# Performance work log

Hardware: AMD Instinct MI355X
Metric: run time of the kernel (lower is better)

The kernel has to match this reference:

```python
import jax, jax.numpy as jnp
import numpy as np

H = 8          # attention heads
HID = 256      # hidden dim
C = HID // H   # per-head channels
N = 50000      # nodes per node type
E = 500000     # edges per edge type
LRELU_SLOPE = 0.2
EPS_SOFTMAX = 1e-16
EPS_LN = 1e-5


def _gat(x_src, x_dst, ei, W, a_s, a_d, b, n_dst):
    # PyG GATConv (shared lin for src/dst since in_channels is int), concat heads
    h_src = (x_src @ W).reshape(-1, H, C)   # (Nsrc, H, C)
    h_dst = (x_dst @ W).reshape(-1, H, C)   # (Ndst, H, C)
    al_s = (h_src * a_s).sum(-1)            # (Nsrc, H)
    al_d = (h_dst * a_d).sum(-1)            # (Ndst, H)
    src, dst = ei[0], ei[1]
    alpha = jax.nn.leaky_relu(al_s[src] + al_d[dst], LRELU_SLOPE)  # (E, H)
    # segment softmax over edges grouped by destination node
    amax = jax.ops.segment_max(alpha, dst, num_segments=n_dst)
    amax = jnp.where(jnp.isfinite(amax), amax, 0.0)
    ex = jnp.exp(alpha - amax[dst])
    den = jax.ops.segment_sum(ex, dst, num_segments=n_dst)
    w = ex / (den[dst] + EPS_SOFTMAX)
    msg = h_src[src] * w[:, :, None]        # (E, H, C)
    out = jax.ops.segment_sum(msg, dst, num_segments=n_dst)
    return out.reshape(n_dst, HID) + b


def _ln(x, g, b):
    mu = x.mean(-1, keepdims=True)
    var = x.var(-1, keepdims=True)
    return (x - mu) / jnp.sqrt(var + EPS_LN) * g + b


def setup_inputs() -> dict:
    key = jax.random.key(0)
    ks = jax.random.split(key, 24)
    s = 1.0 / np.sqrt(HID)
    d = {}
    d["x_gene"] = jax.random.normal(ks[0], (N, HID), jnp.float32)
    d["x_pheno"] = jax.random.normal(ks[1], (N, HID), jnp.float32)
    d["ei_gp"] = jax.random.randint(ks[2], (2, E), 0, N, jnp.int32)
    d["ei_pg"] = jax.random.randint(ks[3], (2, E), 0, N, jnp.int32)
    d["ei_gg"] = jax.random.randint(ks[4], (2, E), 0, N, jnp.int32)
    i = 5
    for tag in ["gp", "pg", "gg"]:
        d[f"W_{tag}"] = jax.random.normal(ks[i], (HID, HID), jnp.float32) * s; i += 1
        d[f"a_s_{tag}"] = jax.random.normal(ks[i], (H, C), jnp.float32) * s; i += 1
        d[f"a_d_{tag}"] = jax.random.normal(ks[i], (H, C), jnp.float32) * s; i += 1
        d[f"b_{tag}"] = jnp.zeros((HID,), jnp.float32); i += 1
    d["ln_g_gene"] = jnp.ones((HID,), jnp.float32)
    d["ln_b_gene"] = jnp.zeros((HID,), jnp.float32)
    d["ln_g_ph"] = jnp.ones((HID,), jnp.float32)
    d["ln_b_ph"] = jnp.zeros((HID,), jnp.float32)
    return d


def reference(x_gene, x_pheno, ei_gp, ei_pg, ei_gg,
              W_gp, a_s_gp, a_d_gp, b_gp,
              W_pg, a_s_pg, a_d_pg, b_pg,
              W_gg, a_s_gg, a_d_gg, b_gg,
              ln_g_gene, ln_b_gene, ln_g_ph, ln_b_ph):
    # HeteroConv aggr='sum': sum conv outputs per destination node type
    out_gene = (_gat(x_pheno, x_gene, ei_pg, W_pg, a_s_pg, a_d_pg, b_pg, N)
                + _gat(x_gene, x_gene, ei_gg, W_gg, a_s_gg, a_d_gg, b_gg, N))
    out_ph = _gat(x_gene, x_pheno, ei_gp, W_gp, a_s_gp, a_d_gp, b_gp, N)
    # residual + layernorm (dropout is identity in eval / p=0)
    out_gene = _ln(out_gene + x_gene, ln_g_gene, ln_b_gene)
    out_ph = _ln(out_ph + x_pheno, ln_g_ph, ln_b_ph)
    return (out_gene, out_ph)
```

## Files before the change

kernel.cpp:

```cpp
#include <hip/hip_runtime.h>

#define NN 50000
#define EE 500000
#define CAP 64

typedef unsigned int u32;
typedef unsigned short ushort;
typedef __attribute__((ext_vector_type(8))) short short8v;
typedef __attribute__((ext_vector_type(4))) float float4v;

__device__ __forceinline__ ushort f2b(float f) {
  u32 u = __float_as_uint(f);
  u32 r = (u + 0x7fffu + ((u >> 16) & 1u)) >> 16;
  return (ushort)r;
}
__device__ __forceinline__ u32 pk2(float a, float b) {
  return (u32)f2b(a) | ((u32)f2b(b) << 16);
}
__device__ __forceinline__ float bl(u32 q) { return __uint_as_float(q << 16); }
__device__ __forceinline__ float bh(u32 q) { return __uint_as_float(q & 0xffff0000u); }
__device__ __forceinline__ void gload16(const void* g, void* l) {
  __builtin_amdgcn_global_load_lds((const __attribute__((address_space(1))) void*)g,
                                   (__attribute__((address_space(3))) void*)l, 16, 0, 0);
}

__global__ void prep_kernel(const float* __restrict__ W_gp, const float* __restrict__ W_pg,
                            const float* __restrict__ W_gg,
                            const float* __restrict__ as_gp, const float* __restrict__ as_pg,
                            const float* __restrict__ as_gg,
                            const float* __restrict__ ad_gp, const float* __restrict__ ad_pg,
                            const float* __restrict__ ad_gg,
                            const float* __restrict__ xg, const float* __restrict__ xp,
                            ushort* __restrict__ WT, ushort* __restrict__ V6T,
                            ushort* __restrict__ xb, int* __restrict__ cnt3) {
  int b = blockIdx.x;
  int k = threadIdx.x;
  if (b < 256) {
    int n = b;
    WT[(size_t)0 * 65536 + n * 256 + k] = f2b(W_gp[k * 256 + n]);
    WT[(size_t)1 * 65536 + n * 256 + k] = f2b(W_pg[k * 256 + n]);
    WT[(size_t)2 * 65536 + n * 256 + k] = f2b(W_gg[k * 256 + n]);
    return;
  }
  if (b < 304) {
    int idx = b - 256;
    int g = idx >> 3, h = idx & 7;
    const float* W;
    const float* a;
    switch (g) {
      case 0: W = W_gp; a = as_gp; break;
      case 1: W = W_gg; a = as_gg; break;
      case 2: W = W_pg; a = ad_pg; break;
      case 3: W = W_gg; a = ad_gg; break;
      case 4: W = W_pg; a = as_pg; break;
      default: W = W_gp; a = ad_gp; break;
    }
    const float4* wrow = (const float4*)&W[(size_t)k * 256 + h * 32];
    const float4* arow = (const float4*)&a[h * 32];
    float s = 0.f;
#pragma unroll
    for (int q = 0; q < 8; ++q) {
      float4 wv = wrow[q];
      float4 av = arow[q];
      s += wv.x * av.x + wv.y * av.y + wv.z * av.z + wv.w * av.w;
    }
    V6T[(size_t)(g * 8 + h) * 256 + k] = f2b(s);
    return;
  }
  if (b == 304) {
#pragma unroll
    for (int col = 48; col < 64; ++col) V6T[(size_t)col * 256 + k] = 0;
    return;
  }
  int gid = (b - 305) * 256 + k;
  const int gstride = 2048 * 256;
  for (int j = gid; j < 3 * NN; j += gstride) cnt3[j] = 0;
  const int tot = 2 * NN * 64;
  for (int i = gid; i < tot; i += gstride) {
    const float* src = (i < NN * 64) ? xg + (size_t)i * 4 : xp + ((size_t)i - (size_t)NN * 64) * 4;
    float4 v = *(const float4*)src;
    ushort4 o;
    o.x = f2b(v.x); o.y = f2b(v.y); o.z = f2b(v.z); o.w = f2b(v.w);
    *(ushort4*)&xb[(size_t)i * 4] = o;
  }
}

__global__ __launch_bounds__(256) void fused_compute(
    const ushort* __restrict__ xb, const ushort* __restrict__ WT,
    const ushort* __restrict__ V6T, ushort* __restrict__ hb3,
    ushort* __restrict__ alsb, float* __restrict__ ald3,
    const int* __restrict__ e0, const int* __restrict__ e1, const int* __restrict__ e2,
    int* __restrict__ cnt3, ushort* __restrict__ srcs3) {
  __shared__ ushort smem[16384];
  const int tid = threadIdx.x;
  const int l = tid & 63, w = tid >> 6;
  const int rr = l & 15, kb = l >> 4;
  if (blockIdx.y == 0) {
    const int T = 391 * 256;
    const int base = blockIdx.x * 256 + tid;
#pragma unroll
    for (int it = 0; it < 15; ++it) {
      int i = base + it * T;
      if (i < 3 * EE) {
        int which = i >= 2 * EE ? 2 : (i >= EE ? 1 : 0);
        const int* ei = which == 0 ? e0 : (which == 1 ? e1 : e2);
        int e = i - which * EE;
        int d = ei[EE + e];
        int s = ei[e];
        int gslot = which * NN + d;
        int pos = atomicAdd(&cnt3[gslot], 1);
        if (pos < CAP) srcs3[(size_t)gslot * CAP + pos] = (ushort)s;
      }
    }
    return;
  }
  if (blockIdx.y < 7) {
    ushort* As = smem;
    ushort* Bs = smem + 8192;
    const int yy = blockIdx.y - 1;
    const int p = yy >> 1;
    const int c0 = (yy & 1) * 128;
    const ushort* x = xb + (p == 1 ? (size_t)NN * 256 : 0);
    const ushort* Wp = WT + (size_t)p * 65536 + (size_t)c0 * 256;
    ushort* hb = hb3 + (size_t)p * 12800000;
    const int r0 = blockIdx.x * 128;
    const int wm = w >> 1, wn = w & 1;
    float4v acc[4][4];
#pragma unroll
    for (int mi = 0; mi < 4; ++mi)
#pragma unroll
      for (int ni = 0; ni < 4; ++ni) acc[mi][ni] = (float4v){0.f, 0.f, 0.f, 0.f};
    const int r1 = tid >> 2, g1 = tid & 3;
    const int r2 = 64 + (tid >> 2), g2 = tid & 3;

#define STAGE(buf, k0)                                                               \
  {                                                                                  \
    gload16(&x[(size_t)(r0 + r1) * 256 + (k0) + g1 * 8], &As[(buf) * 4096 + tid * 8]); \
    gload16(&x[(size_t)(r0 + r2) * 256 + (k0) + g2 * 8], &As[(buf) * 4096 + (tid + 256) * 8]); \
    gload16(&Wp[(size_t)r1 * 256 + (k0) + g1 * 8], &Bs[(buf) * 4096 + tid * 8]);     \
    gload16(&Wp[(size_t)r2 * 256 + (k0) + g2 * 8], &Bs[(buf) * 4096 + (tid + 256) * 8]); \
  }

    STAGE(0, 0);
    __syncthreads();
#pragma unroll
    for (int k = 0; k < 8; ++k) {
      const int buf = k & 1;
      if (k < 7) STAGE(buf ^ 1, (k + 1) * 32);
      short8v af[4], bf[4];
#pragma unroll
      for (int t = 0; t < 4; ++t) {
        af[t] = *(const short8v*)&As[buf * 4096 + (wm * 64 + t * 16 + rr) * 32 + kb * 8];
        bf[t] = *(const short8v*)&Bs[buf * 4096 + (wn * 64 + t * 16 + rr) * 32 + kb * 8];
      }
#pragma unroll
      for (int mi = 0; mi < 4; ++mi)
#pragma unroll
        for (int ni = 0; ni < 4; ++ni)
          acc[mi][ni] = __builtin_amdgcn_mfma_f32_16x16x32_bf16(bf[ni], af[mi], acc[mi][ni], 0, 0, 0);
      __syncthreads();
    }
#undef STAGE
#pragma unroll
    for (int mi = 0; mi < 4; ++mi) {
      const int row = r0 + wm * 64 + mi * 16 + rr;
      if (row < NN) {
        ushort* hp = &hb[(size_t)row * 256 + c0 + wn * 64 + kb * 4];
#pragma unroll
        for (int ni = 0; ni < 4; ++ni) {
          uint2 o;
          o.x = pk2(acc[mi][ni][0], acc[mi][ni][1]);
          o.y = pk2(acc[mi][ni][2], acc[mi][ni][3]);
          *(uint2*)&hp[ni * 16] = o;
        }
      }
    }
    return;
  }
  ushort* As2 = smem;
  short8v bfv[8];
#pragma unroll
  for (int k = 0; k < 8; ++k) {
    uint4 q = *(const uint4*)&V6T[(size_t)(w * 16 + rr) * 256 + k * 32 + kb * 8];
    bfv[k] = *(short8v*)&q;
  }
  for (int t = 0; t < 4; ++t) {
    const int r0 = blockIdx.x * 256 + t * 64;
    gload16(&xb[(size_t)(r0 + (tid >> 2)) * 256 + (tid & 3) * 8], &As2[tid * 8]);
    __syncthreads();
    float4v acc[4];
#pragma unroll
    for (int mi = 0; mi < 4; ++mi) acc[mi] = (float4v){0.f, 0.f, 0.f, 0.f};
#pragma unroll
    for (int k = 0; k < 8; ++k) {
      const int buf = k & 1;
      if (k < 7)
        gload16(&xb[(size_t)(r0 + (tid >> 2)) * 256 + (k + 1) * 32 + (tid & 3) * 8],
                &As2[(buf ^ 1) * 2048 + tid * 8]);
#pragma unroll
      for (int mi = 0; mi < 4; ++mi) {
        short8v afv = *(const short8v*)&As2[buf * 2048 + (mi * 16 + rr) * 32 + kb * 8];
        acc[mi] = __builtin_amdgcn_mfma_f32_16x16x32_bf16(bfv[k], afv, acc[mi], 0, 0, 0);
      }
      __syncthreads();
    }
    const int g = w * 2 + (kb >> 1);
    const int idx = (kb & 1) * 4;
#pragma unroll
    for (int mi = 0; mi < 4; ++mi) {
      int grow = r0 + mi * 16 + rr;
      float4 val = make_float4(acc[mi][0], acc[mi][1], acc[mi][2], acc[mi][3]);
      if (grow < NN) {
        if (g == 0 || g == 1) {
          ushort* arr = alsb + (g == 0 ? 0 : 800000);
          uint2 o;
          o.x = pk2(val.x, val.y);
          o.y = pk2(val.z, val.w);
          *(uint2*)&arr[(size_t)grow * 8 + idx] = o;
        } else if (g == 2 || g == 3) {
          float* arr = ald3 + (g == 2 ? 400000 : 800000);
          *(float4*)&arr[(size_t)grow * 8 + idx] = val;
        }
      } else if (grow < 2 * NN) {
        int r = grow - NN;
        if (g == 4) {
          uint2 o;
          o.x = pk2(val.x, val.y);
          o.y = pk2(val.z, val.w);
          *(uint2*)&alsb[400000 + (size_t)r * 8 + idx] = o;
        } else if (g == 5) {
          *(float4*)&ald3[(size_t)r * 8 + idx] = val;
        }
      }
    }
  }
}

__global__ __launch_bounds__(256) void gat_gather_ln(
    const int* __restrict__ cnt3, const ushort* __restrict__ srcs3,
    const ushort* __restrict__ hb3, const ushort* __restrict__ alsb,
    const float* __restrict__ ald3, const ushort* __restrict__ xb,
    const float* __restrict__ b_gp, const float* __restrict__ b_pg,
    const float* __restrict__ b_gg,
    const float* __restrict__ lng_g, const float* __restrict__ lnb_g,
    const float* __restrict__ lng_p, const float* __restrict__ lnb_p,
    float* __restrict__ out) {
  __shared__ float exs[4][8][68];
  __shared__ int ssrc[4][64];
  const int l = threadIdx.x & 63;
  const int wv = threadIdx.x >> 6;
  const int slot = blockIdx.x * 4 + wv;
  if (slot >= 2 * NN) return;
  const bool gene = (slot < NN);
  const int d = gene ? slot : slot - NN;
  const int sl = l & 31;
  const int half = l >> 5;
  const int hh = sl >> 2;
  float vout[8] = {0.f, 0.f, 0.f, 0.f, 0.f, 0.f, 0.f, 0.f};
  const int nph = gene ? 2 : 1;
  for (int q = 0; q < nph; ++q) {
    const int phase = gene ? (1 + q) : 0;
    const int cslot = phase * NN + d;
    const ushort* hmat = hb3 + (size_t)phase * 12800000;
    const ushort* al_s = alsb + (size_t)phase * 400000;
    const float* al_d = ald3 + (size_t)phase * 400000;
    const int cnt = cnt3[cslot];
    if (cnt == 0) continue;
    const ushort* srow = srcs3 + (size_t)cslot * CAP;
    float4 ad0 = *(const float4*)&al_d[(size_t)d * 8];
    float4 ad1 = *(const float4*)&al_d[(size_t)d * 8 + 4];
    const float ald[8] = {ad0.x, ad0.y, ad0.z, ad0.w, ad1.x, ad1.y, ad1.z, ad1.w};
    float den = 0.f;
    float acc8[8] = {0.f, 0.f, 0.f, 0.f, 0.f, 0.f, 0.f, 0.f};
    const ushort* hrow = hmat + sl * 8;
    {
      float ex[8] = {0.f, 0.f, 0.f, 0.f, 0.f, 0.f, 0.f, 0.f};
      int s = 0;
      if (l < cnt) {
        s = srow[l];
        uint4 sq = *(const uint4*)&al_s[(size_t)s * 8];
        float a[8] = {bl(sq.x) + ald[0], bh(sq.x) + ald[1], bl(sq.y) + ald[2], bh(sq.y) + ald[3],
                      bl(sq.z) + ald[4], bh(sq.z) + ald[5], bl(sq.w) + ald[6], bh(sq.w) + ald[7]};
#pragma unroll
        for (int h = 0; h < 8; ++h) ex[h] = __expf(fmaxf(a[h], 0.2f * a[h]));
      }
      ssrc[wv][l] = s;
#pragma unroll
      for (int h = 0; h < 8; ++h) exs[wv][h][l] = ex[h];
      int chunkr = (cnt + 3) & ~3;
      for (int j = 0; j < chunkr; j += 4) {
        int ja = j + half, jb = j + 2 + half;
        int sa = ssrc[wv][ja], sb = ssrc[wv][jb];
        float wa = exs[wv][hh][ja], wb = exs[wv][hh][jb];
        uint4 pa = *(const uint4*)&hrow[(size_t)sa * 256];
        uint4 pb = *(const uint4*)&hrow[(size_t)sb * 256];
        den += wa + wb;
        acc8[0] += bl(pa.x) * wa + bl(pb.x) * wb;
        acc8[1] += bh(pa.x) * wa + bh(pb.x) * wb;
        acc8[2] += bl(pa.y) * wa + bl(pb.y) * wb;
        acc8[3] += bh(pa.y) * wa + bh(pb.y) * wb;
        acc8[4] += bl(pa.z) * wa + bl(pb.z) * wb;
        acc8[5] += bh(pa.z) * wa + bh(pb.z) * wb;
        acc8[6] += bl(pa.w) * wa + bl(pb.w) * wb;
        acc8[7] += bh(pa.w) * wa + bh(pb.w) * wb;
      }
    }
#pragma unroll
    for (int i = 0; i < 8; ++i) acc8[i] += __shfl_xor(acc8[i], 32);
    den += __shfl_xor(den, 32);
    float wd = 1.f / (den + 1e-16f);
#pragma unroll
    for (int i = 0; i < 8; ++i) vout[i] += acc8[i] * wd;
  }
  const ushort* xrow = xb + (gene ? 0 : (size_t)NN * 256) + (size_t)d * 256;
  uint4 xq = *(const uint4*)&xrow[sl * 8];
  float4 ba, bb;
  if (gene) {
    float4 p1 = *(const float4*)&b_pg[sl * 8];
    float4 p2 = *(const float4*)&b_pg[sl * 8 + 4];
    float4 q1 = *(const float4*)&b_gg[sl * 8];
    float4 q2 = *(const float4*)&b_gg[sl * 8 + 4];
    ba = make_float4(p1.x + q1.x, p1.y + q1.y, p1.z + q1.z, p1.w + q1.w);
    bb = make_float4(p2.x + q2.x, p2.y + q2.y, p2.z + q2.z, p2.w + q2.w);
  } else {
    ba = *(const float4*)&b_gp[sl * 8];
    bb = *(const float4*)&b_gp[sl * 8 + 4];
  }
  vout[0] += bl(xq.x) + ba.x; vout[1] += bh(xq.x) + ba.y;
  vout[2] += bl(xq.y) + ba.z; vout[3] += bh(xq.y) + ba.w;
  vout[4] += bl(xq.z) + bb.x; vout[5] += bh(xq.z) + bb.y;
  vout[6] += bl(xq.w) + bb.z; vout[7] += bh(xq.w) + bb.w;
  float s = 0.f, ss = 0.f;
#pragma unroll
  for (int i = 0; i < 8; ++i) { s += vout[i]; ss += vout[i] * vout[i]; }
#pragma unroll
  for (int off = 1; off < 32; off <<= 1) {
    s += __shfl_xor(s, off);
    ss += __shfl_xor(ss, off);
  }
  float mu = s * (1.f / 256.f);
  float var = ss * (1.f / 256.f) - mu * mu;
  float rstd = rsqrtf(var + 1e-5f);
  const float* lg = gene ? lng_g : lng_p;
  const float* lb = gene ? lnb_g : lnb_p;
  float4 g1 = *(const float4*)&lg[sl * 8];
  float4 g2 = *(const float4*)&lg[sl * 8 + 4];
  float4 c1 = *(const float4*)&lb[sl * 8];
  float4 c2 = *(const float4*)&lb[sl * 8 + 4];
  if (half == 0) {
    float* op = &out[(size_t)slot * 256 + sl * 8];
    float4 o1 = make_float4((vout[0] - mu) * rstd * g1.x + c1.x,
                            (vout[1] - mu) * rstd * g1.y + c1.y,
                            (vout[2] - mu) * rstd * g1.z + c1.z,
                            (vout[3] - mu) * rstd * g1.w + c1.w);
    float4 o2 = make_float4((vout[4] - mu) * rstd * g2.x + c2.x,
                            (vout[5] - mu) * rstd * g2.y + c2.y,
                            (vout[6] - mu) * rstd * g2.z + c2.z,
                            (vout[7] - mu) * rstd * g2.w + c2.w);
    *(float4*)op = o1;
    *(float4*)(op + 4) = o2;
  }
}

extern "C" void kernel_launch(void* const* d_in, const int* in_sizes, int n_in,
                              void* d_out, int out_size, void* d_ws, size_t ws_size,
                              hipStream_t stream) {
  const float* x_gene = (const float*)d_in[0];
  const float* x_pheno = (const float*)d_in[1];
  const int* ei_gp = (const int*)d_in[2];
  const int* ei_pg = (const int*)d_in[3];
  const int* ei_gg = (const int*)d_in[4];
  const float* W_gp = (const float*)d_in[5];
  const float* a_s_gp = (const float*)d_in[6];
  const float* a_d_gp = (const float*)d_in[7];
  const float* b_gp = (const float*)d_in[8];
  const float* W_pg = (const float*)d_in[9];
  const float* a_s_pg = (const float*)d_in[10];
  const float* a_d_pg = (const float*)d_in[11];
  const float* b_pg = (const float*)d_in[12];
  const float* W_gg = (const float*)d_in[13];
  const float* a_s_gg = (const float*)d_in[14];
  const float* a_d_gg = (const float*)d_in[15];
  const float* b_gg = (const float*)d_in[16];
  const float* ln_g_gene = (const float*)d_in[17];
  const float* ln_b_gene = (const float*)d_in[18];
  const float* ln_g_ph = (const float*)d_in[19];
  const float* ln_b_ph = (const float*)d_in[20];
  float* out = (float*)d_out;

  float* ws = (float*)d_ws;
  ushort* hb3 = (ushort*)ws;
  ushort* xb = (ushort*)(ws + 19200000);
  ushort* alsb = (ushort*)(ws + 32060000);
  float* ald3 = ws + 32700000;
  ushort* WT = (ushort*)(ws + 33960000);
  ushort* V6T = (ushort*)(ws + 34060000);
  int* ibase = (int*)(ws + 34080000);
  int* cnt3 = ibase;
  ushort* srcs3 = (ushort*)(ibase + 150016);

  prep_kernel<<<305 + 2048, 256, 0, stream>>>(
      W_gp, W_pg, W_gg, a_s_gp, a_s_pg, a_s_gg, a_d_gp, a_d_pg, a_d_gg,
      x_gene, x_pheno, WT, V6T, xb, cnt3);

  fused_compute<<<dim3(391, 8), 256, 0, stream>>>(xb, WT, V6T, hb3, alsb, ald3,
                                                  ei_gp, ei_pg, ei_gg, cnt3, srcs3);

  gat_gather_ln<<<(2 * NN + 3) / 4, 256, 0, stream>>>(
      cnt3, srcs3, hb3, alsb, ald3, xb, b_gp, b_pg, b_gg,
      ln_g_gene, ln_b_gene, ln_g_ph, ln_b_ph, out);
}
```

Baseline: 298.8 us.

## Move edge bucketing into prep kernel and zero counters with memset

Measured after the change: 336.5 us. +12.6%, slower.

```diff
diff --git a/kernel.cpp b/kernel.cpp
--- a/kernel.cpp
+++ b/kernel.cpp
@@ -31,8 +31,11 @@
                             const float* __restrict__ ad_gp, const float* __restrict__ ad_pg,
                             const float* __restrict__ ad_gg,
                             const float* __restrict__ xg, const float* __restrict__ xp,
+                            const int* __restrict__ e0, const int* __restrict__ e1,
+                            const int* __restrict__ e2,
                             ushort* __restrict__ WT, ushort* __restrict__ V6T,
-                            ushort* __restrict__ xb, int* __restrict__ cnt3) {
+                            ushort* __restrict__ xb, int* __restrict__ cnt3,
+                            ushort* __restrict__ srcs3) {
   int b = blockIdx.x;
   int k = threadIdx.x;
   if (b < 256) {
@@ -72,52 +75,43 @@
     for (int col = 48; col < 64; ++col) V6T[(size_t)col * 256 + k] = 0;
     return;
   }
-  int gid = (b - 305) * 256 + k;
-  const int gstride = 2048 * 256;
-  for (int j = gid; j < 3 * NN; j += gstride) cnt3[j] = 0;
-  const int tot = 2 * NN * 64;
-  for (int i = gid; i < tot; i += gstride) {
-    const float* src = (i < NN * 64) ? xg + (size_t)i * 4 : xp + ((size_t)i - (size_t)NN * 64) * 4;
-    float4 v = *(const float4*)src;
-    ushort4 o;
-    o.x = f2b(v.x); o.y = f2b(v.y); o.z = f2b(v.z); o.w = f2b(v.w);
-    *(ushort4*)&xb[(size_t)i * 4] = o;
-  }
-}
-
-__global__ __launch_bounds__(256) void fused_compute(
+  if (b < 2353) {
+    int i = (b - 305) * 256 + k;
+    const int gstride = 2048 * 256;
+    const int tot = 2 * NN * 64;
+    for (; i < tot; i += gstride) {
+      const float* src = (i < NN * 64) ? xg + (size_t)i * 4 : xp + ((size_t)i - (size_t)NN * 64) * 4;
+      float4 v = *(const float4*)src;
+      ushort4 o;
+      o.x = f2b(v.x); o.y = f2b(v.y); o.z = f2b(v.z); o.w = f2b(v.w);
+      *(ushort4*)&xb[(size_t)i * 4] = o;
+    }
+    return;
+  }
+  int i = (b - 2353) * 256 + k;
+  if (i >= 3 * EE) return;
+  int which = i >= 2 * EE ? 2 : (i >= EE ? 1 : 0);
+  const int* ei = which == 0 ? e0 : (which == 1 ? e1 : e2);
+  int e = i - which * EE;
+  int d = ei[EE + e];
+  int s = ei[e];
+  int gslot = which * NN + d;
+  int pos = atomicAdd(&cnt3[gslot], 1);
+  if (pos < CAP) srcs3[(size_t)gslot * CAP + pos] = (ushort)s;
+}
+
+__global__ __launch_bounds__(256) void compute_kernel(
     const ushort* __restrict__ xb, const ushort* __restrict__ WT,
     const ushort* __restrict__ V6T, ushort* __restrict__ hb3,
-    ushort* __restrict__ alsb, float* __restrict__ ald3,
-    const int* __restrict__ e0, const int* __restrict__ e1, const int* __restrict__ e2,
-    int* __restrict__ cnt3, ushort* __restrict__ srcs3) {
+    ushort* __restrict__ alsb, float* __restrict__ ald3) {
   __shared__ ushort smem[16384];
   const int tid = threadIdx.x;
   const int l = tid & 63, w = tid >> 6;
   const int rr = l & 15, kb = l >> 4;
-  if (blockIdx.y == 0) {
-    const int T = 391 * 256;
-    const int base = blockIdx.x * 256 + tid;
-#pragma unroll
-    for (int it = 0; it < 15; ++it) {
-      int i = base + it * T;
-      if (i < 3 * EE) {
-        int which = i >= 2 * EE ? 2 : (i >= EE ? 1 : 0);
-        const int* ei = which == 0 ? e0 : (which == 1 ? e1 : e2);
-        int e = i - which * EE;
-        int d = ei[EE + e];
-        int s = ei[e];
-        int gslot = which * NN + d;
-        int pos = atomicAdd(&cnt3[gslot], 1);
-        if (pos < CAP) srcs3[(size_t)gslot * CAP + pos] = (ushort)s;
-      }
-    }
-    return;
-  }
-  if (blockIdx.y < 7) {
+  if (blockIdx.y < 6) {
     ushort* As = smem;
     ushort* Bs = smem + 8192;
-    const int yy = blockIdx.y - 1;
+    const int yy = blockIdx.y;
     const int p = yy >> 1;
     const int c0 = (yy & 1) * 128;
     const ushort* x = xb + (p == 1 ? (size_t)NN * 256 : 0);
@@ -399,12 +393,14 @@
   int* cnt3 = ibase;
   ushort* srcs3 = (ushort*)(ibase + 150016);
 
-  prep_kernel<<<305 + 2048, 256, 0, stream>>>(
+  const int e3blk = (3 * EE + 255) / 256;
+
+  hipMemsetAsync(cnt3, 0, 150016 * 4, stream);
+  prep_kernel<<<2353 + e3blk, 256, 0, stream>>>(
       W_gp, W_pg, W_gg, a_s_gp, a_s_pg, a_s_gg, a_d_gp, a_d_pg, a_d_gg,
-      x_gene, x_pheno, WT, V6T, xb, cnt3);
-
-  fused_compute<<<dim3(391, 8), 256, 0, stream>>>(xb, WT, V6T, hb3, alsb, ald3,
-                                                  ei_gp, ei_pg, ei_gg, cnt3, srcs3);
+      x_gene, x_pheno, ei_gp, ei_pg, ei_gg, WT, V6T, xb, cnt3, srcs3);
+
+  compute_kernel<<<dim3(391, 7), 256, 0, stream>>>(xb, WT, V6T, hb3, alsb, ald3);
 
   gat_gather_ln<<<(2 * NN + 3) / 4, 256, 0, stream>>>(
       cnt3, srcs3, hb3, alsb, ald3, xb, b_gp, b_pg, b_gg,
```

## Fuse fp32-to-bf16 input conversion into GEMM staging and drop xb buffer

Applied to the files above, without the earlier changes.

Result: no change. 299.7 us (+0.3%).

```diff
diff --git a/kernel.cpp b/kernel.cpp
--- a/kernel.cpp
+++ b/kernel.cpp
@@ -30,9 +30,7 @@
                             const float* __restrict__ as_gg,
                             const float* __restrict__ ad_gp, const float* __restrict__ ad_pg,
                             const float* __restrict__ ad_gg,
-                            const float* __restrict__ xg, const float* __restrict__ xp,
-                            ushort* __restrict__ WT, ushort* __restrict__ V6T,
-                            ushort* __restrict__ xb, int* __restrict__ cnt3) {
+                            ushort* __restrict__ WT, ushort* __restrict__ V6T) {
   int b = blockIdx.x;
   int k = threadIdx.x;
   if (b < 256) {
@@ -67,28 +65,14 @@
     V6T[(size_t)(g * 8 + h) * 256 + k] = f2b(s);
     return;
   }
-  if (b == 304) {
-#pragma unroll
-    for (int col = 48; col < 64; ++col) V6T[(size_t)col * 256 + k] = 0;
-    return;
-  }
-  int gid = (b - 305) * 256 + k;
-  const int gstride = 2048 * 256;
-  for (int j = gid; j < 3 * NN; j += gstride) cnt3[j] = 0;
-  const int tot = 2 * NN * 64;
-  for (int i = gid; i < tot; i += gstride) {
-    const float* src = (i < NN * 64) ? xg + (size_t)i * 4 : xp + ((size_t)i - (size_t)NN * 64) * 4;
-    float4 v = *(const float4*)src;
-    ushort4 o;
-    o.x = f2b(v.x); o.y = f2b(v.y); o.z = f2b(v.z); o.w = f2b(v.w);
-    *(ushort4*)&xb[(size_t)i * 4] = o;
-  }
-}
-
-__global__ __launch_bounds__(256) void fused_compute(
-    const ushort* __restrict__ xb, const ushort* __restrict__ WT,
-    const ushort* __restrict__ V6T, ushort* __restrict__ hb3,
-    ushort* __restrict__ alsb, float* __restrict__ ald3,
+#pragma unroll
+  for (int col = 48; col < 64; ++col) V6T[(size_t)col * 256 + k] = 0;
+}
+
+__global__ __launch_bounds__(256) void mega_compute(
+    const float* __restrict__ xg, const float* __restrict__ xp,
+    const ushort* __restrict__ WT, const ushort* __restrict__ V6T,
+    ushort* __restrict__ hb3, ushort* __restrict__ alsb, float* __restrict__ ald3,
     const int* __restrict__ e0, const int* __restrict__ e1, const int* __restrict__ e2,
     int* __restrict__ cnt3, ushort* __restrict__ srcs3) {
   __shared__ ushort smem[16384];
@@ -120,7 +104,7 @@
     const int yy = blockIdx.y - 1;
     const int p = yy >> 1;
     const int c0 = (yy & 1) * 128;
-    const ushort* x = xb + (p == 1 ? (size_t)NN * 256 : 0);
+    const float* x = (p == 1) ? xp : xg;
     const ushort* Wp = WT + (size_t)p * 65536 + (size_t)c0 * 256;
     ushort* hb = hb3 + (size_t)p * 12800000;
     const int r0 = blockIdx.x * 128;
@@ -130,15 +114,31 @@
     for (int mi = 0; mi < 4; ++mi)
 #pragma unroll
       for (int ni = 0; ni < 4; ++ni) acc[mi][ni] = (float4v){0.f, 0.f, 0.f, 0.f};
-    const int r1 = tid >> 2, g1 = tid & 3;
-    const int r2 = 64 + (tid >> 2), g2 = tid & 3;
+    const int ra = r0 + (tid >> 2);
+    const int rb = r0 + 64 + (tid >> 2);
+    const int ko = (tid & 3) * 8;
+    const bool oka = (ra < NN), okb = (rb < NN);
+    const float* pa_ = &x[(size_t)(oka ? ra : 0) * 256 + ko];
+    const float* pb_ = &x[(size_t)(okb ? rb : 0) * 256 + ko];
 
 #define STAGE(buf, k0)                                                               \
   {                                                                                  \
-    gload16(&x[(size_t)(r0 + r1) * 256 + (k0) + g1 * 8], &As[(buf) * 4096 + tid * 8]); \
-    gload16(&x[(size_t)(r0 + r2) * 256 + (k0) + g2 * 8], &As[(buf) * 4096 + (tid + 256) * 8]); \
-    gload16(&Wp[(size_t)r1 * 256 + (k0) + g1 * 8], &Bs[(buf) * 4096 + tid * 8]);     \
-    gload16(&Wp[(size_t)r2 * 256 + (k0) + g2 * 8], &Bs[(buf) * 4096 + (tid + 256) * 8]); \
+    uint4 qa = make_uint4(0u, 0u, 0u, 0u), qb = qa;                                  \
+    if (oka) {                                                                       \
+      float4 f0 = *(const float4*)(pa_ + (k0));                                      \
+      float4 f1 = *(const float4*)(pa_ + (k0) + 4);                                  \
+      qa = make_uint4(pk2(f0.x, f0.y), pk2(f0.z, f0.w), pk2(f1.x, f1.y), pk2(f1.z, f1.w)); \
+    }                                                                                \
+    if (okb) {                                                                       \
+      float4 f0 = *(const float4*)(pb_ + (k0));                                      \
+      float4 f1 = *(const float4*)(pb_ + (k0) + 4);                                  \
+      qb = make_uint4(pk2(f0.x, f0.y), pk2(f0.z, f0.w), pk2(f1.x, f1.y), pk2(f1.z, f1.w)); \
+    }                                                                                \
+    *(uint4*)&As[(buf) * 4096 + tid * 8] = qa;                                       \
+    *(uint4*)&As[(buf) * 4096 + (tid + 256) * 8] = qb;                               \
+    gload16(&Wp[(size_t)(tid >> 2) * 256 + (k0) + ko], &Bs[(buf) * 4096 + tid * 8]); \
+    gload16(&Wp[(size_t)(64 + (tid >> 2)) * 256 + (k0) + ko],                        \
+            &Bs[(buf) * 4096 + (tid + 256) * 8]);                                    \
   }
 
     STAGE(0, 0);
@@ -184,9 +184,23 @@
     uint4 q = *(const uint4*)&V6T[(size_t)(w * 16 + rr) * 256 + k * 32 + kb * 8];
     bfv[k] = *(short8v*)&q;
   }
+  const int ko = (tid & 3) * 8;
   for (int t = 0; t < 4; ++t) {
     const int r0 = blockIdx.x * 256 + t * 64;
-    gload16(&xb[(size_t)(r0 + (tid >> 2)) * 256 + (tid & 3) * 8], &As2[tid * 8]);
+    const int row = r0 + (tid >> 2);
+    const float* xr = row < NN ? &xg[(size_t)row * 256 + ko]
+                    : (row < 2 * NN ? &xp[(size_t)(row - NN) * 256 + ko] : nullptr);
+#define STAGEA(buf, k0)                                                              \
+  {                                                                                  \
+    uint4 q = make_uint4(0u, 0u, 0u, 0u);                                            \
+    if (xr) {                                                                        \
+      float4 f0 = *(const float4*)(xr + (k0));                                       \
+      float4 f1 = *(const float4*)(xr + (k0) + 4);                                   \
+      q = make_uint4(pk2(f0.x, f0.y), pk2(f0.z, f0.w), pk2(f1.x, f1.y), pk2(f1.z, f1.w)); \
+    }                                                                                \
+    *(uint4*)&As2[(buf) * 2048 + tid * 8] = q;                                       \
+  }
+    STAGEA(0, 0);
     __syncthreads();
     float4v acc[4];
 #pragma unroll
@@ -194,9 +208,7 @@
 #pragma unroll
     for (int k = 0; k < 8; ++k) {
       const int buf = k & 1;
-      if (k < 7)
-        gload16(&xb[(size_t)(r0 + (tid >> 2)) * 256 + (k + 1) * 32 + (tid & 3) * 8],
-                &As2[(buf ^ 1) * 2048 + tid * 8]);
+      if (k < 7) STAGEA(buf ^ 1, (k + 1) * 32);
 #pragma unroll
       for (int mi = 0; mi < 4; ++mi) {
         short8v afv = *(const short8v*)&As2[buf * 2048 + (mi * 16 + rr) * 32 + kb * 8];
@@ -204,6 +216,7 @@
       }
       __syncthreads();
     }
+#undef STAGEA
     const int g = w * 2 + (kb >> 1);
     const int idx = (kb & 1) * 4;
 #pragma unroll
@@ -239,7 +252,8 @@
 __global__ __launch_bounds__(256) void gat_gather_ln(
     const int* __restrict__ cnt3, const ushort* __restrict__ srcs3,
     const ushort* __restrict__ hb3, const ushort* __restrict__ alsb,
-    const float* __restrict__ ald3, const ushort* __restrict__ xb,
+    const float* __restrict__ ald3,
+    const float* __restrict__ xg, const float* __restrict__ xp,
     const float* __restrict__ b_gp, const float* __restrict__ b_pg,
     const float* __restrict__ b_gg,
     const float* __restrict__ lng_g, const float* __restrict__ lnb_g,
@@ -312,8 +326,9 @@
 #pragma unroll
     for (int i = 0; i < 8; ++i) vout[i] += acc8[i] * wd;
   }
-  const ushort* xrow = xb + (gene ? 0 : (size_t)NN * 256) + (size_t)d * 256;
-  uint4 xq = *(const uint4*)&xrow[sl * 8];
+  const float* xrow = (gene ? xg : xp) + (size_t)d * 256;
+  float4 xa = *(const float4*)&xrow[sl * 8];
+  float4 xc = *(const float4*)&xrow[sl * 8 + 4];
   float4 ba, bb;
   if (gene) {
     float4 p1 = *(const float4*)&b_pg[sl * 8];
@@ -326,10 +341,10 @@
     ba = *(const float4*)&b_gp[sl * 8];
     bb = *(const float4*)&b_gp[sl * 8 + 4];
   }
-  vout[0] += bl(xq.x) + ba.x; vout[1] += bh(xq.x) + ba.y;
-  vout[2] += bl(xq.y) + ba.z; vout[3] += bh(xq.y) + ba.w;
-  vout[4] += bl(xq.z) + bb.x; vout[5] += bh(xq.z) + bb.y;
-  vout[6] += bl(xq.w) + bb.z; vout[7] += bh(xq.w) + bb.w;
+  vout[0] += xa.x + ba.x; vout[1] += xa.y + ba.y;
+  vout[2] += xa.z + ba.z; vout[3] += xa.w + ba.w;
+  vout[4] += xc.x + bb.x; vout[5] += xc.y + bb.y;
+  vout[6] += xc.z + bb.z; vout[7] += xc.w + bb.w;
   float s = 0.f, ss = 0.f;
 #pragma unroll
   for (int i = 0; i < 8; ++i) { s += vout[i]; ss += vout[i] * vout[i]; }
@@ -390,23 +405,22 @@
 
   float* ws = (float*)d_ws;
   ushort* hb3 = (ushort*)ws;
-  ushort* xb = (ushort*)(ws + 19200000);
-  ushort* alsb = (ushort*)(ws + 32060000);
-  float* ald3 = ws + 32700000;
-  ushort* WT = (ushort*)(ws + 33960000);
-  ushort* V6T = (ushort*)(ws + 34060000);
-  int* ibase = (int*)(ws + 34080000);
+  ushort* alsb = (ushort*)(ws + 19200000);
+  float* ald3 = ws + 19840000;
+  ushort* WT = (ushort*)(ws + 21100000);
+  ushort* V6T = (ushort*)(ws + 21200000);
+  int* ibase = (int*)(ws + 21220000);
   int* cnt3 = ibase;
   ushort* srcs3 = (ushort*)(ibase + 150016);
 
-  prep_kernel<<<305 + 2048, 256, 0, stream>>>(
-      W_gp, W_pg, W_gg, a_s_gp, a_s_pg, a_s_gg, a_d_gp, a_d_pg, a_d_gg,
-      x_gene, x_pheno, WT, V6T, xb, cnt3);
-
-  fused_compute<<<dim3(391, 8), 256, 0, stream>>>(xb, WT, V6T, hb3, alsb, ald3,
-                                                  ei_gp, ei_pg, ei_gg, cnt3, srcs3);
+  hipMemsetAsync(cnt3, 0, 150016 * 4, stream);
+  prep_kernel<<<305, 256, 0, stream>>>(W_gp, W_pg, W_gg, a_s_gp, a_s_pg, a_s_gg,
+                                       a_d_gp, a_d_pg, a_d_gg, WT, V6T);
+
+  mega_compute<<<dim3(391, 8), 256, 0, stream>>>(
+      x_gene, x_pheno, WT, V6T, hb3, alsb, ald3, ei_gp, ei_pg, ei_gg, cnt3, srcs3);
 
   gat_gather_ln<<<(2 * NN + 3) / 4, 256, 0, stream>>>(
-      cnt3, srcs3, hb3, alsb, ald3, xb, b_gp, b_pg, b_gg,
+      cnt3, srcs3, hb3, alsb, ald3, x_gene, x_pheno, b_gp, b_pg, b_gg,
       ln_g_gene, ln_b_gene, ln_g_ph, ln_b_ph, out);
 }
```
